# Optimization experiments

Measured on AMD Instinct MI355X. Metric: run time of the kernel, lower is better.

Reference implementation:

```python
import jax, jax.numpy as jnp
import numpy as np

N_NODES = 100000
N_EDGES = 2000000
N_GRAPHS = 1000
DIM = 32
NUM_FEATURES = 7
NUM_CLASSES = 2
BN_EPS = 1e-5


def setup_inputs() -> dict:
    key = jax.random.key(0)
    ks = jax.random.split(key, 24)
    inp = {
        "x": jax.random.normal(ks[0], (N_NODES, NUM_FEATURES), dtype=jnp.float32),
        "edge_index": jax.random.randint(ks[1], (2, N_EDGES), 0, N_NODES, dtype=jnp.int64),
        "batch": jnp.sort(jax.random.randint(ks[2], (N_NODES,), 0, N_GRAPHS, dtype=jnp.int64)),
        "conv1_W1": jax.random.normal(ks[3], (NUM_FEATURES, DIM), dtype=jnp.float32) * 0.3,
        "conv1_b1": jax.random.normal(ks[4], (DIM,), dtype=jnp.float32) * 0.1,
        "conv1_W2": jax.random.normal(ks[5], (DIM, DIM), dtype=jnp.float32) * 0.15,
        "conv1_b2": jax.random.normal(ks[6], (DIM,), dtype=jnp.float32) * 0.1,
        "convs_W1": jax.random.normal(ks[7], (4, DIM, DIM), dtype=jnp.float32) * 0.15,
        "convs_b1": jax.random.normal(ks[8], (4, DIM), dtype=jnp.float32) * 0.1,
        "convs_W2": jax.random.normal(ks[9], (4, DIM, DIM), dtype=jnp.float32) * 0.15,
        "convs_b2": jax.random.normal(ks[10], (4, DIM), dtype=jnp.float32) * 0.1,
        "bn_gamma": jax.random.uniform(ks[11], (5, DIM), dtype=jnp.float32, minval=0.5, maxval=1.5),
        "bn_beta": jax.random.normal(ks[12], (5, DIM), dtype=jnp.float32) * 0.1,
        "bn_mean": jax.random.normal(ks[13], (5, DIM), dtype=jnp.float32) * 0.1,
        "bn_var": jax.random.uniform(ks[14], (5, DIM), dtype=jnp.float32, minval=0.5, maxval=1.5),
        "fc1_W": jax.random.normal(ks[15], (DIM, DIM), dtype=jnp.float32) * 0.15,
        "fc1_b": jax.random.normal(ks[16], (DIM,), dtype=jnp.float32) * 0.1,
        "fc2_W": jax.random.normal(ks[17], (DIM, NUM_CLASSES), dtype=jnp.float32) * 0.15,
        "fc2_b": jax.random.normal(ks[18], (NUM_CLASSES,), dtype=jnp.float32) * 0.1,
    }
    return inp


def _gin_conv(h, src, dst, W1, b1, W2, b2):
    # GINConv with eps=0: nn((1+eps)*x + sum_{j in N(i)} x_j)
    agg = jax.ops.segment_sum(h[src], dst, num_segments=N_NODES)
    z = h + agg
    z = jnp.maximum(z @ W1 + b1, 0.0)
    return z @ W2 + b2


def _bn_eval(h, gamma, beta, mean, var):
    return (h - mean) * jax.lax.rsqrt(var + BN_EPS) * gamma + beta


def reference(x, edge_index, batch,
              conv1_W1, conv1_b1, conv1_W2, conv1_b2,
              convs_W1, convs_b1, convs_W2, convs_b2,
              bn_gamma, bn_beta, bn_mean, bn_var,
              fc1_W, fc1_b, fc2_W, fc2_b):
    src, dst = edge_index[0], edge_index[1]
    h = _gin_conv(x, src, dst, conv1_W1, conv1_b1, conv1_W2, conv1_b2)
    h = jnp.maximum(h, 0.0)
    h = _bn_eval(h, bn_gamma[0], bn_beta[0], bn_mean[0], bn_var[0])
    for i in range(4):  # conv2..conv5
        h = _gin_conv(h, src, dst, convs_W1[i], convs_b1[i], convs_W2[i], convs_b2[i])
        h = jnp.maximum(h, 0.0)
        h = _bn_eval(h, bn_gamma[i + 1], bn_beta[i + 1], bn_mean[i + 1], bn_var[i + 1])
    # global add pool over graphs
    g = jax.ops.segment_sum(h, batch, num_segments=N_GRAPHS)  # [G, DIM]
    g = jnp.maximum(g @ fc1_W + fc1_b, 0.0)
    # dropout: eval mode -> identity
    logits = g @ fc2_W + fc2_b
    return jax.nn.log_softmax(logits, axis=-1)
```

## Files before the change

### kernel.cpp

```cpp
#include <hip/hip_runtime.h>

#define N_NODES  100000
#define N_EDGES  2000000
#define N_GRAPHS 1000
#define NFEAT    7
#define BN_EPS   1e-5f
#define MAXDEG   64

#define BSH      7
#define NBKT     782
#define BCAP     3584
#define E_PER_BLK 4096

__device__ __forceinline__ unsigned bf16_rne(float f) {
  unsigned u = __float_as_uint(f);
  return (u + 0x7FFFu + ((u >> 16) & 1u)) >> 16;
}
__device__ __forceinline__ float bf_lo(unsigned u) { return __uint_as_float(u << 16); }
__device__ __forceinline__ float bf_hi(unsigned u) { return __uint_as_float(u & 0xFFFF0000u); }

__global__ __launch_bounds__(1024) void b1_bucket(const int* __restrict__ src,
                                                  const int* __restrict__ dst,
                                                  int* __restrict__ gCur,
                                                  unsigned* __restrict__ ebuf) {
  __shared__ int hist[NBKT], base[NBKT];
  int tid = threadIdx.x;
  for (int i = tid; i < NBKT; i += 1024) hist[i] = 0;
  __syncthreads();
  unsigned pk[4];
  int bo[4];
  int e0 = blockIdx.x * E_PER_BLK;
#pragma unroll
  for (int k = 0; k < 4; ++k) {
    int e = e0 + k * 1024 + tid;
    if (e < N_EDGES) {
      int d = dst[e], s = src[e];
      int b = d >> BSH;
      int off = atomicAdd(&hist[b], 1);
      pk[k] = ((unsigned)(d & 127) << 17) | (unsigned)s;
      bo[k] = (b << 17) | off;
    } else {
      bo[k] = -1;
    }
  }
  __syncthreads();
  for (int i = tid; i < NBKT; i += 1024)
    base[i] = hist[i] ? atomicAdd(&gCur[i], hist[i]) : 0;
  __syncthreads();
#pragma unroll
  for (int k = 0; k < 4; ++k) {
    if (bo[k] >= 0) {
      int b = bo[k] >> 17, off = bo[k] & 0x1FFFF;
      int p = base[b] + off;
      if (p < BCAP) ebuf[(size_t)b * BCAP + p] = pk[k];
    }
  }
}

__global__ __launch_bounds__(512) void b2_csr(const unsigned* __restrict__ ebuf,
                                              const int* __restrict__ gCnt,
                                              int* __restrict__ cnt,
                                              int* __restrict__ csr) {
  __shared__ int hist[128];
  __shared__ int stage[128 * MAXDEG];
  int b = blockIdx.x, tid = threadIdx.x;
  if (tid < 128) hist[tid] = 0;
  __syncthreads();
  int n = gCnt[b];
  if (n > BCAP) n = BCAP;
  const unsigned* eb = ebuf + (size_t)b * BCAP;
  for (int i = tid; i < n; i += 512) {
    unsigned pk = eb[i];
    int dloc = (int)(pk >> 17);
    int slot = atomicAdd(&hist[dloc], 1);
    if (slot < MAXDEG) stage[(dloc << 6) + slot] = (int)(pk & 0x1FFFFu);
  }
  __syncthreads();
  if (tid < 128) {
    int gnode = (b << BSH) + tid;
    if (gnode < N_NODES) cnt[gnode] = hist[tid];
  }
  const int4* st4 = (const int4*)stage;
  int4* dst4 = (int4*)(csr + (size_t)b * (128 * MAXDEG));
  for (int i = tid; i < 128 * MAXDEG / 4; i += 512) dst4[i] = st4[i];
}

__global__ __launch_bounds__(256) void xcvt_kernel(const float* __restrict__ x,
                                                   unsigned* __restrict__ xc) {
  int i = blockIdx.x * 256 + threadIdx.x;
  if (i >= N_NODES * 4) return;
  int n = i >> 2, p = i & 3;
  float lo = x[n * 7 + 2 * p];
  float hi = (2 * p + 1 < 7) ? x[n * 7 + 2 * p + 1] : 0.f;
  xc[i] = bf16_rne(lo) | (bf16_rne(hi) << 16);
}

__global__ __launch_bounds__(256) void gin1(
    const unsigned short* __restrict__ xc16, const int* __restrict__ cnt,
    const int* __restrict__ csr,
    const float* __restrict__ W1, const float* __restrict__ b1,
    const float* __restrict__ W2, const float* __restrict__ b2,
    const float* __restrict__ gamma, const float* __restrict__ beta,
    const float* __restrict__ mean, const float* __restrict__ var,
    unsigned short* __restrict__ hout16) {
  __shared__ __align__(16) float zsA[4][8], zsB[4][8];
  __shared__ __align__(16) float tsA[4][32], tsB[4][32];
  int tid = threadIdx.x;
  int w = __builtin_amdgcn_readfirstlane(tid >> 6);
  int lane = tid & 63;
  int grp = lane >> 2;
  int ch  = lane & 3;
  int half = lane >> 5, j = lane & 31;

  float wr1[4], wr2[16];
#pragma unroll
  for (int i = 0; i < 4; ++i) {
    int k = half * 4 + i;
    wr1[i] = (k < 7) ? W1[k * 32 + j] : 0.f;
  }
#pragma unroll
  for (int i = 0; i < 16; ++i) wr2[i] = W2[(half * 16 + i) * 32 + j];
  float vb1 = b1[j], vb2 = b2[j];
  float sc = gamma[j] * rsqrtf(var[j] + BN_EPS);
  float sh = beta[j] - mean[j] * sc;

  const unsigned* xc32 = (const unsigned*)xc16;

  const int NW = gridDim.x * 4;
  const int NPAIR = N_NODES / 2;
  for (int pr = blockIdx.x * 4 + w; pr < NPAIR; pr += NW) {
    int n0 = 2 * pr, n1 = n0 + 1;
    int d0 = cnt[n0];
    int d1 = cnt[n1];
    if (d0 > 63) d0 = 63;
    if (d1 > 63) d1 = 63;
    int dE0 = d0 + 1, dE1 = d1 + 1;

    int idx0 = (lane < d0) ? csr[n0 * MAXDEG + lane] : n0;
    int idx1 = (lane < d1) ? csr[n1 * MAXDEG + lane] : n1;

    unsigned vA[4], vB[4];
#pragma unroll
    for (int s = 0; s < 4; ++s) {
      int sidA = __shfl(idx0, s * 16 + grp);
      vA[s] = xc32[(size_t)sidA * 4 + ch];
    }
#pragma unroll
    for (int s = 0; s < 4; ++s) {
      int sidB = __shfl(idx1, s * 16 + grp);
      vB[s] = xc32[(size_t)sidB * 4 + ch];
    }

    float a0 = 0.f, a1 = 0.f;
    float c0 = 0.f, c1 = 0.f;
#pragma unroll
    for (int s = 0; s < 4; ++s) {
      int e = s * 16 + grp;
      if (e < dE0) { a0 += bf_lo(vA[s]); a1 += bf_hi(vA[s]); }
      if (e < dE1) { c0 += bf_lo(vB[s]); c1 += bf_hi(vB[s]); }
    }
#pragma unroll
    for (int m = 4; m <= 32; m <<= 1) {
      a0 += __shfl_xor(a0, m); a1 += __shfl_xor(a1, m);
      c0 += __shfl_xor(c0, m); c1 += __shfl_xor(c1, m);
    }
    if (grp == 0) {
      float2 za = {a0, a1};
      float2 zc = {c0, c1};
      *(float2*)&zsA[w][ch * 2] = za;
      *(float2*)&zsB[w][ch * 2] = zc;
    }

    float tp = half ? 0.f : vb1;
    {
      const float4* zp = (const float4*)&zsA[w][half * 4];
      float4 z0 = zp[0];
      tp = fmaf(z0.x, wr1[0], tp); tp = fmaf(z0.y, wr1[1], tp);
      tp = fmaf(z0.z, wr1[2], tp); tp = fmaf(z0.w, wr1[3], tp);
    }
    tp += __shfl_xor(tp, 32);
    tp = fmaxf(tp, 0.f);
    if (!half) tsA[w][j] = tp;

    float op = half ? 0.f : vb2;
    {
      const float4* tpp = (const float4*)&tsA[w][half * 16];
      float4 t0 = tpp[0], t1 = tpp[1], t2 = tpp[2], t3 = tpp[3];
      op = fmaf(t0.x, wr2[0], op);  op = fmaf(t0.y, wr2[1], op);
      op = fmaf(t0.z, wr2[2], op);  op = fmaf(t0.w, wr2[3], op);
      op = fmaf(t1.x, wr2[4], op);  op = fmaf(t1.y, wr2[5], op);
      op = fmaf(t1.z, wr2[6], op);  op = fmaf(t1.w, wr2[7], op);
      op = fmaf(t2.x, wr2[8], op);  op = fmaf(t2.y, wr2[9], op);
      op = fmaf(t2.z, wr2[10], op); op = fmaf(t2.w, wr2[11], op);
      op = fmaf(t3.x, wr2[12], op); op = fmaf(t3.y, wr2[13], op);
      op = fmaf(t3.z, wr2[14], op); op = fmaf(t3.w, wr2[15], op);
    }
    op += __shfl_xor(op, 32);
    if (!half) {
      op = fmaxf(op, 0.f) * sc + sh;
      float hi = __shfl(op, j | 1);
      if ((j & 1) == 0) {
        unsigned pk = bf16_rne(op) | (bf16_rne(hi) << 16);
        ((unsigned*)hout16)[n0 * 16 + (j >> 1)] = pk;
      }
    }

    float tq = half ? 0.f : vb1;
    {
      const float4* zp = (const float4*)&zsB[w][half * 4];
      float4 z0 = zp[0];
      tq = fmaf(z0.x, wr1[0], tq); tq = fmaf(z0.y, wr1[1], tq);
      tq = fmaf(z0.z, wr1[2], tq); tq = fmaf(z0.w, wr1[3], tq);
    }
    tq += __shfl_xor(tq, 32);
    tq = fmaxf(tq, 0.f);
    if (!half) tsB[w][j] = tq;

    float oq = half ? 0.f : vb2;
    {
      const float4* tpp = (const float4*)&tsB[w][half * 16];
      float4 t0 = tpp[0], t1 = tpp[1], t2 = tpp[2], t3 = tpp[3];
      oq = fmaf(t0.x, wr2[0], oq);  oq = fmaf(t0.y, wr2[1], oq);
      oq = fmaf(t0.z, wr2[2], oq);  oq = fmaf(t0.w, wr2[3], oq);
      oq = fmaf(t1.x, wr2[4], oq);  oq = fmaf(t1.y, wr2[5], oq);
      oq = fmaf(t1.z, wr2[6], oq);  oq = fmaf(t1.w, wr2[7], oq);
      oq = fmaf(t2.x, wr2[8], oq);  oq = fmaf(t2.y, wr2[9], oq);
      oq = fmaf(t2.z, wr2[10], oq); oq = fmaf(t2.w, wr2[11], oq);
      oq = fmaf(t3.x, wr2[12], oq); oq = fmaf(t3.y, wr2[13], oq);
      oq = fmaf(t3.z, wr2[14], oq); oq = fmaf(t3.w, wr2[15], oq);
    }
    oq += __shfl_xor(oq, 32);
    if (!half) {
      oq = fmaxf(oq, 0.f) * sc + sh;
      float hi = __shfl(oq, j | 1);
      if ((j & 1) == 0) {
        unsigned pk = bf16_rne(oq) | (bf16_rne(hi) << 16);
        ((unsigned*)hout16)[n1 * 16 + (j >> 1)] = pk;
      }
    }
  }
}

__global__ __launch_bounds__(256) void gin_layer32(
    const unsigned short* __restrict__ hin16, const int* __restrict__ cnt,
    const int* __restrict__ csr,
    const float* __restrict__ W1, const float* __restrict__ b1,
    const float* __restrict__ W2, const float* __restrict__ b2,
    const float* __restrict__ gamma, const float* __restrict__ beta,
    const float* __restrict__ mean, const float* __restrict__ var,
    unsigned short* __restrict__ hout16) {
  __shared__ __align__(16) float zsA[4][32], tsA[4][32];
  __shared__ __align__(16) float zsB[4][32], tsB[4][32];
  int tid = threadIdx.x;
  int w = __builtin_amdgcn_readfirstlane(tid >> 6);
  int lane = tid & 63;
  int grp = lane >> 3;
  int ch  = lane & 7;
  int half = lane >> 5, j = lane & 31;

  float wr1[16], wr2[16];
#pragma unroll
  for (int i = 0; i < 16; ++i) wr1[i] = W1[(half * 16 + i) * 32 + j];
#pragma unroll
  for (int i = 0; i < 16; ++i) wr2[i] = W2[(half * 16 + i) * 32 + j];
  float vb1 = b1[j], vb2 = b2[j];
  float sc = gamma[j] * rsqrtf(var[j] + BN_EPS);
  float sh = beta[j] - mean[j] * sc;

  const int NW = gridDim.x * 4;
  const int NPAIR = N_NODES / 2;
  for (int pr = blockIdx.x * 4 + w; pr < NPAIR; pr += NW) {
    int n0 = 2 * pr, n1 = n0 + 1;
    int d0 = cnt[n0];
    int d1 = cnt[n1];
    if (d0 > 63) d0 = 63;
    if (d1 > 63) d1 = 63;
    int dE0 = d0 + 1, dE1 = d1 + 1;

    int idx0 = (lane < d0) ? csr[n0 * MAXDEG + lane] : n0;
    int idx1 = (lane < d1) ? csr[n1 * MAXDEG + lane] : n1;

    uint2 vA[8], vB[8];
#pragma unroll
    for (int s = 0; s < 8; ++s) {
      int sidA = __shfl(idx0, s * 8 + grp);
      vA[s] = *(const uint2*)(hin16 + (size_t)sidA * 32 + ch * 4);
    }
#pragma unroll
    for (int s = 0; s < 8; ++s) {
      int sidB = __shfl(idx1, s * 8 + grp);
      vB[s] = *(const uint2*)(hin16 + (size_t)sidB * 32 + ch * 4);
    }

    float a0 = 0.f, a1 = 0.f, a2 = 0.f, a3 = 0.f;
    float c0 = 0.f, c1 = 0.f, c2 = 0.f, c3 = 0.f;
#pragma unroll
    for (int s = 0; s < 8; ++s) {
      int e = s * 8 + grp;
      if (e < dE0) {
        a0 += bf_lo(vA[s].x); a1 += bf_hi(vA[s].x);
        a2 += bf_lo(vA[s].y); a3 += bf_hi(vA[s].y);
      }
      if (e < dE1) {
        c0 += bf_lo(vB[s].x); c1 += bf_hi(vB[s].x);
        c2 += bf_lo(vB[s].y); c3 += bf_hi(vB[s].y);
      }
    }
#pragma unroll
    for (int m = 8; m <= 32; m <<= 1) {
      a0 += __shfl_xor(a0, m); a1 += __shfl_xor(a1, m);
      a2 += __shfl_xor(a2, m); a3 += __shfl_xor(a3, m);
      c0 += __shfl_xor(c0, m); c1 += __shfl_xor(c1, m);
      c2 += __shfl_xor(c2, m); c3 += __shfl_xor(c3, m);
    }
    if (grp == 0) {
      float4 za = {a0, a1, a2, a3};
      float4 zc = {c0, c1, c2, c3};
      *(float4*)&zsA[w][ch * 4] = za;
      *(float4*)&zsB[w][ch * 4] = zc;
    }

    float tp = half ? 0.f : vb1;
    {
      const float4* zp = (const float4*)&zsA[w][half * 16];
      float4 q0 = zp[0], q1 = zp[1], q2 = zp[2], q3 = zp[3];
      tp = fmaf(q0.x, wr1[0], tp);  tp = fmaf(q0.y, wr1[1], tp);
      tp = fmaf(q0.z, wr1[2], tp);  tp = fmaf(q0.w, wr1[3], tp);
      tp = fmaf(q1.x, wr1[4], tp);  tp = fmaf(q1.y, wr1[5], tp);
      tp = fmaf(q1.z, wr1[6], tp);  tp = fmaf(q1.w, wr1[7], tp);
      tp = fmaf(q2.x, wr1[8], tp);  tp = fmaf(q2.y, wr1[9], tp);
      tp = fmaf(q2.z, wr1[10], tp); tp = fmaf(q2.w, wr1[11], tp);
      tp = fmaf(q3.x, wr1[12], tp); tp = fmaf(q3.y, wr1[13], tp);
      tp = fmaf(q3.z, wr1[14], tp); tp = fmaf(q3.w, wr1[15], tp);
    }
    tp += __shfl_xor(tp, 32);
    tp = fmaxf(tp, 0.f);
    if (!half) tsA[w][j] = tp;

    float op = half ? 0.f : vb2;
    {
      const float4* tpp = (const float4*)&tsA[w][half * 16];
      float4 q0 = tpp[0], q1 = tpp[1], q2 = tpp[2], q3 = tpp[3];
      op = fmaf(q0.x, wr2[0], op);  op = fmaf(q0.y, wr2[1], op);
      op = fmaf(q0.z, wr2[2], op);  op = fmaf(q0.w, wr2[3], op);
      op = fmaf(q1.x, wr2[4], op);  op = fmaf(q1.y, wr2[5], op);
      op = fmaf(q1.z, wr2[6], op);  op = fmaf(q1.w, wr2[7], op);
      op = fmaf(q2.x, wr2[8], op);  op = fmaf(q2.y, wr2[9], op);
      op = fmaf(q2.z, wr2[10], op); op = fmaf(q2.w, wr2[11], op);
      op = fmaf(q3.x, wr2[12], op); op = fmaf(q3.y, wr2[13], op);
      op = fmaf(q3.z, wr2[14], op); op = fmaf(q3.w, wr2[15], op);
    }
    op += __shfl_xor(op, 32);
    if (!half) {
      op = fmaxf(op, 0.f) * sc + sh;
      float hi = __shfl(op, j | 1);
      if ((j & 1) == 0) {
        unsigned pk = bf16_rne(op) | (bf16_rne(hi) << 16);
        ((unsigned*)hout16)[n0 * 16 + (j >> 1)] = pk;
      }
    }

    float tq = half ? 0.f : vb1;
    {
      const float4* zp = (const float4*)&zsB[w][half * 16];
      float4 q0 = zp[0], q1 = zp[1], q2 = zp[2], q3 = zp[3];
      tq = fmaf(q0.x, wr1[0], tq);  tq = fmaf(q0.y, wr1[1], tq);
      tq = fmaf(q0.z, wr1[2], tq);  tq = fmaf(q0.w, wr1[3], tq);
      tq = fmaf(q1.x, wr1[4], tq);  tq = fmaf(q1.y, wr1[5], tq);
      tq = fmaf(q1.z, wr1[6], tq);  tq = fmaf(q1.w, wr1[7], tq);
      tq = fmaf(q2.x, wr1[8], tq);  tq = fmaf(q2.y, wr1[9], tq);
      tq = fmaf(q2.z, wr1[10], tq); tq = fmaf(q2.w, wr1[11], tq);
      tq = fmaf(q3.x, wr1[12], tq); tq = fmaf(q3.y, wr1[13], tq);
      tq = fmaf(q3.z, wr1[14], tq); tq = fmaf(q3.w, wr1[15], tq);
    }
    tq += __shfl_xor(tq, 32);
    tq = fmaxf(tq, 0.f);
    if (!half) tsB[w][j] = tq;

    float oq = half ? 0.f : vb2;
    {
      const float4* tpp = (const float4*)&tsB[w][half * 16];
      float4 q0 = tpp[0], q1 = tpp[1], q2 = tpp[2], q3 = tpp[3];
      oq = fmaf(q0.x, wr2[0], oq);  oq = fmaf(q0.y, wr2[1], oq);
      oq = fmaf(q0.z, wr2[2], oq);  oq = fmaf(q0.w, wr2[3], oq);
      oq = fmaf(q1.x, wr2[4], oq);  oq = fmaf(q1.y, wr2[5], oq);
      oq = fmaf(q1.z, wr2[6], oq);  oq = fmaf(q1.w, wr2[7], oq);
      oq = fmaf(q2.x, wr2[8], oq);  oq = fmaf(q2.y, wr2[9], oq);
      oq = fmaf(q2.z, wr2[10], oq); oq = fmaf(q2.w, wr2[11], oq);
      oq = fmaf(q3.x, wr2[12], oq); oq = fmaf(q3.y, wr2[13], oq);
      oq = fmaf(q3.z, wr2[14], oq); oq = fmaf(q3.w, wr2[15], oq);
    }
    oq += __shfl_xor(oq, 32);
    if (!half) {
      oq = fmaxf(oq, 0.f) * sc + sh;
      float hi = __shfl(oq, j | 1);
      if ((j & 1) == 0) {
        unsigned pk = bf16_rne(oq) | (bf16_rne(hi) << 16);
        ((unsigned*)hout16)[n1 * 16 + (j >> 1)] = pk;
      }
    }
  }
}

__global__ __launch_bounds__(256) void pool_kernel(const unsigned short* __restrict__ h16,
                                                   const int* __restrict__ batch,
                                                   float* __restrict__ g) {
  __shared__ int s_lo, s_hi;
  __shared__ float red[8][33];
  int gr = blockIdx.x;
  if (threadIdx.x == 0) {
    int lo = 0, hi = N_NODES;
    while (lo < hi) { int m = (lo + hi) >> 1; if (batch[m] < gr) lo = m + 1; else hi = m; }
    s_lo = lo;
  } else if (threadIdx.x == 1) {
    int lo = 0, hi = N_NODES;
    while (lo < hi) { int m = (lo + hi) >> 1; if (batch[m] < gr + 1) lo = m + 1; else hi = m; }
    s_hi = lo;
  }
  __syncthreads();
  int lo = s_lo, hi = s_hi;
  int j = threadIdx.x & 31;
  int nd = threadIdx.x >> 5;
  float acc = 0.f;
  for (int n = lo + nd; n < hi; n += 8)
    acc += __uint_as_float((unsigned)h16[n * 32 + j] << 16);
  red[nd][j] = acc;
  __syncthreads();
  if (threadIdx.x < 32) {
    float s = 0.f;
#pragma unroll
    for (int r = 0; r < 8; ++r) s += red[r][j];
    g[gr * 32 + j] = s;
  }
}

__global__ __launch_bounds__(256) void head_kernel(
    const float* __restrict__ g, const float* __restrict__ W1, const float* __restrict__ b1,
    const float* __restrict__ W2, const float* __restrict__ b2, float* __restrict__ out) {
  __shared__ float sW1[1024], sb1[32];
  __shared__ float sW2[64], sb2[2];
  __shared__ float zb[8][33], tb[8][33], lb[8][2];
  int tid = threadIdx.x;
  for (int i = tid; i < 1024; i += 256) sW1[i] = W1[i];
  if (tid < 64) sW2[tid] = W2[tid];
  if (tid < 32) sb1[tid] = b1[tid];
  if (tid < 2) sb2[tid] = b2[tid];
  int nd = tid >> 5;
  int gr = blockIdx.x * 8 + nd;
  int j = tid & 31;
  __syncthreads();
  float z = (gr < N_GRAPHS) ? g[gr * 32 + j] : 0.f;
  zb[nd][j] = z;
  __syncthreads();
  float t = sb1[j];
#pragma unroll
  for (int k = 0; k < 32; ++k) t = fmaf(zb[nd][k], sW1[k * 32 + j], t);
  t = fmaxf(t, 0.f);
  tb[nd][j] = t;
  __syncthreads();
  if (j < 2) {
    float l = sb2[j];
#pragma unroll
    for (int k = 0; k < 32; ++k) l = fmaf(tb[nd][k], sW2[k * 2 + j], l);
    lb[nd][j] = l;
  }
  __syncthreads();
  if (gr < N_GRAPHS && j < 2) {
    float l0 = lb[nd][0], l1 = lb[nd][1];
    float m = fmaxf(l0, l1);
    float lse = m + logf(expf(l0 - m) + expf(l1 - m));
    out[gr * 2 + j] = lb[nd][j] - lse;
  }
}

extern "C" void kernel_launch(void* const* d_in, const int* in_sizes, int n_in,
                              void* d_out, int out_size, void* d_ws, size_t ws_size,
                              hipStream_t stream) {
  const float* x     = (const float*)d_in[0];
  const int*   eidx  = (const int*)d_in[1];
  const int*   batch = (const int*)d_in[2];
  const float* c1W1  = (const float*)d_in[3];
  const float* c1b1  = (const float*)d_in[4];
  const float* c1W2  = (const float*)d_in[5];
  const float* c1b2  = (const float*)d_in[6];
  const float* csW1  = (const float*)d_in[7];
  const float* csb1  = (const float*)d_in[8];
  const float* csW2  = (const float*)d_in[9];
  const float* csb2  = (const float*)d_in[10];
  const float* bng   = (const float*)d_in[11];
  const float* bnb   = (const float*)d_in[12];
  const float* bnm   = (const float*)d_in[13];
  const float* bnv   = (const float*)d_in[14];
  const float* fc1W  = (const float*)d_in[15];
  const float* fc1b  = (const float*)d_in[16];
  const float* fc2W  = (const float*)d_in[17];
  const float* fc2b  = (const float*)d_in[18];
  float* out = (float*)d_out;

  const int* src = eidx;
  const int* dst = eidx + N_EDGES;

  char* p = (char*)d_ws;
  unsigned short* hA16 = (unsigned short*)p; p += (size_t)N_NODES * 32 * 2;
  unsigned short* hB16 = (unsigned short*)p; p += (size_t)N_NODES * 32 * 2;
  int*      cnt  = (int*)p;      p += (size_t)N_NODES * 4;
  int*      csr  = (int*)p;      p += (size_t)NBKT * 128 * MAXDEG * 4;
  unsigned* ebuf = (unsigned*)p; p += (size_t)NBKT * BCAP * 4;
  int*      gCur = (int*)p;      p += 1024 * 4;
  float*    g    = (float*)p;    p += (size_t)N_GRAPHS * 32 * 4;
  unsigned* xc = ebuf;

  hipMemsetAsync(gCur, 0, 1024 * 4, stream);
  b1_bucket<<<(N_EDGES + E_PER_BLK - 1) / E_PER_BLK, 1024, 0, stream>>>(src, dst, gCur, ebuf);
  b2_csr<<<NBKT, 512, 0, stream>>>(ebuf, gCur, cnt, csr);

  xcvt_kernel<<<(N_NODES * 4 + 255) / 256, 256, 0, stream>>>(x, xc);

  gin1<<<2048, 256, 0, stream>>>(
      (const unsigned short*)xc, cnt, csr, c1W1, c1b1, c1W2, c1b2,
      bng, bnb, bnm, bnv, hA16);

  unsigned short* cur = hA16;
  unsigned short* nxt = hB16;
  for (int i = 0; i < 4; ++i) {
    gin_layer32<<<2048, 256, 0, stream>>>(
        cur, cnt, csr,
        csW1 + (size_t)i * 1024, csb1 + (size_t)i * 32,
        csW2 + (size_t)i * 1024, csb2 + (size_t)i * 32,
        bng + (size_t)(i + 1) * 32, bnb + (size_t)(i + 1) * 32,
        bnm + (size_t)(i + 1) * 32, bnv + (size_t)(i + 1) * 32, nxt);
    unsigned short* tmp = cur; cur = nxt; nxt = tmp;
  }

  pool_kernel<<<N_GRAPHS, 256, 0, stream>>>(cur, batch, g);
  head_kernel<<<(N_GRAPHS + 7) / 8, 256, 0, stream>>>(g, fc1W, fc1b, fc2W, fc2b, out);
}
```

Measured before the change: 366.3 us.

## Split GIN layer into separate aggregation and MLP kernels via fp32 buffer

The fused gather-plus-MLP layer kernel is split into an aggregation kernel that writes fp32 z rows to a global buffer and a tiled MLP kernel that processes 64 nodes per block from shared memory. Dropping the weight registers from the gather kernel is meant to improve occupancy and latency hiding for the irregular neighbor loads. In exchange, each layer adds an fp32 write and read of the full node-feature matrix plus an extra launch. Workspace buffers are re-aliased so the z buffer reuses the edge-bucket scratch.

```diff
diff --git a/kernel.cpp b/kernel.cpp
--- a/kernel.cpp
+++ b/kernel.cpp
@@ -241,31 +241,14 @@
   }
 }
 
-__global__ __launch_bounds__(256) void gin_layer32(
+__global__ __launch_bounds__(256) void gin32_agg(
     const unsigned short* __restrict__ hin16, const int* __restrict__ cnt,
-    const int* __restrict__ csr,
-    const float* __restrict__ W1, const float* __restrict__ b1,
-    const float* __restrict__ W2, const float* __restrict__ b2,
-    const float* __restrict__ gamma, const float* __restrict__ beta,
-    const float* __restrict__ mean, const float* __restrict__ var,
-    unsigned short* __restrict__ hout16) {
-  __shared__ __align__(16) float zsA[4][32], tsA[4][32];
-  __shared__ __align__(16) float zsB[4][32], tsB[4][32];
+    const int* __restrict__ csr, float* __restrict__ z) {
   int tid = threadIdx.x;
   int w = __builtin_amdgcn_readfirstlane(tid >> 6);
   int lane = tid & 63;
   int grp = lane >> 3;
   int ch  = lane & 7;
-  int half = lane >> 5, j = lane & 31;
-
-  float wr1[16], wr2[16];
-#pragma unroll
-  for (int i = 0; i < 16; ++i) wr1[i] = W1[(half * 16 + i) * 32 + j];
-#pragma unroll
-  for (int i = 0; i < 16; ++i) wr2[i] = W2[(half * 16 + i) * 32 + j];
-  float vb1 = b1[j], vb2 = b2[j];
-  float sc = gamma[j] * rsqrtf(var[j] + BN_EPS);
-  float sh = beta[j] - mean[j] * sc;
 
   const int NW = gridDim.x * 4;
   const int NPAIR = N_NODES / 2;
@@ -316,13 +299,55 @@
     if (grp == 0) {
       float4 za = {a0, a1, a2, a3};
       float4 zc = {c0, c1, c2, c3};
-      *(float4*)&zsA[w][ch * 4] = za;
-      *(float4*)&zsB[w][ch * 4] = zc;
-    }
-
+      *(float4*)(z + (size_t)n0 * 32 + ch * 4) = za;
+      *(float4*)(z + (size_t)n1 * 32 + ch * 4) = zc;
+    }
+  }
+}
+
+__global__ __launch_bounds__(256) void mlp32(
+    const float* __restrict__ z,
+    const float* __restrict__ W1, const float* __restrict__ b1,
+    const float* __restrict__ W2, const float* __restrict__ b2,
+    const float* __restrict__ gamma, const float* __restrict__ beta,
+    const float* __restrict__ mean, const float* __restrict__ var,
+    unsigned short* __restrict__ hout16) {
+  __shared__ __align__(16) float zs[64][36];
+  __shared__ __align__(16) float ts[4][32];
+  int tid = threadIdx.x;
+  int w = __builtin_amdgcn_readfirstlane(tid >> 6);
+  int lane = tid & 63;
+  int half = lane >> 5, j = lane & 31;
+
+  float wr1[16], wr2[16];
+#pragma unroll
+  for (int i = 0; i < 16; ++i) wr1[i] = W1[(half * 16 + i) * 32 + j];
+#pragma unroll
+  for (int i = 0; i < 16; ++i) wr2[i] = W2[(half * 16 + i) * 32 + j];
+  float vb1 = b1[j], vb2 = b2[j];
+  float sc = gamma[j] * rsqrtf(var[j] + BN_EPS);
+  float sh = beta[j] - mean[j] * sc;
+
+  int base = blockIdx.x * 64;
+  {
+    int r = tid >> 2, c = (tid & 3) * 8;
+    int node = base + r;
+    float4 f0 = {0.f, 0.f, 0.f, 0.f}, f1 = f0;
+    if (node < N_NODES) {
+      const float4* zp = (const float4*)(z + (size_t)node * 32 + c);
+      f0 = zp[0]; f1 = zp[1];
+    }
+    *(float4*)&zs[r][c]     = f0;
+    *(float4*)&zs[r][c + 4] = f1;
+  }
+  __syncthreads();
+
+  for (int p = 0; p < 16; ++p) {
+    int nloc = (w << 4) + p;
+    int node = base + nloc;
     float tp = half ? 0.f : vb1;
     {
-      const float4* zp = (const float4*)&zsA[w][half * 16];
+      const float4* zp = (const float4*)&zs[nloc][half * 16];
       float4 q0 = zp[0], q1 = zp[1], q2 = zp[2], q3 = zp[3];
       tp = fmaf(q0.x, wr1[0], tp);  tp = fmaf(q0.y, wr1[1], tp);
       tp = fmaf(q0.z, wr1[2], tp);  tp = fmaf(q0.w, wr1[3], tp);
@@ -335,11 +360,10 @@
     }
     tp += __shfl_xor(tp, 32);
     tp = fmaxf(tp, 0.f);
-    if (!half) tsA[w][j] = tp;
-
+    if (!half) ts[w][j] = tp;
     float op = half ? 0.f : vb2;
     {
-      const float4* tpp = (const float4*)&tsA[w][half * 16];
+      const float4* tpp = (const float4*)&ts[w][half * 16];
       float4 q0 = tpp[0], q1 = tpp[1], q2 = tpp[2], q3 = tpp[3];
       op = fmaf(q0.x, wr2[0], op);  op = fmaf(q0.y, wr2[1], op);
       op = fmaf(q0.z, wr2[2], op);  op = fmaf(q0.w, wr2[3], op);
@@ -351,52 +375,12 @@
       op = fmaf(q3.z, wr2[14], op); op = fmaf(q3.w, wr2[15], op);
     }
     op += __shfl_xor(op, 32);
-    if (!half) {
+    if (!half && node < N_NODES) {
       op = fmaxf(op, 0.f) * sc + sh;
       float hi = __shfl(op, j | 1);
       if ((j & 1) == 0) {
         unsigned pk = bf16_rne(op) | (bf16_rne(hi) << 16);
-        ((unsigned*)hout16)[n0 * 16 + (j >> 1)] = pk;
-      }
-    }
-
-    float tq = half ? 0.f : vb1;
-    {
-      const float4* zp = (const float4*)&zsB[w][half * 16];
-      float4 q0 = zp[0], q1 = zp[1], q2 = zp[2], q3 = zp[3];
-      tq = fmaf(q0.x, wr1[0], tq);  tq = fmaf(q0.y, wr1[1], tq);
-      tq = fmaf(q0.z, wr1[2], tq);  tq = fmaf(q0.w, wr1[3], tq);
-      tq = fmaf(q1.x, wr1[4], tq);  tq = fmaf(q1.y, wr1[5], tq);
-      tq = fmaf(q1.z, wr1[6], tq);  tq = fmaf(q1.w, wr1[7], tq);
-      tq = fmaf(q2.x, wr1[8], tq);  tq = fmaf(q2.y, wr1[9], tq);
-      tq = fmaf(q2.z, wr1[10], tq); tq = fmaf(q2.w, wr1[11], tq);
-      tq = fmaf(q3.x, wr1[12], tq); tq = fmaf(q3.y, wr1[13], tq);
-      tq = fmaf(q3.z, wr1[14], tq); tq = fmaf(q3.w, wr1[15], tq);
-    }
-    tq += __shfl_xor(tq, 32);
-    tq = fmaxf(tq, 0.f);
-    if (!half) tsB[w][j] = tq;
-
-    float oq = half ? 0.f : vb2;
-    {
-      const float4* tpp = (const float4*)&tsB[w][half * 16];
-      float4 q0 = tpp[0], q1 = tpp[1], q2 = tpp[2], q3 = tpp[3];
-      oq = fmaf(q0.x, wr2[0], oq);  oq = fmaf(q0.y, wr2[1], oq);
-      oq = fmaf(q0.z, wr2[2], oq);  oq = fmaf(q0.w, wr2[3], oq);
-      oq = fmaf(q1.x, wr2[4], oq);  oq = fmaf(q1.y, wr2[5], oq);
-      oq = fmaf(q1.z, wr2[6], oq);  oq = fmaf(q1.w, wr2[7], oq);
-      oq = fmaf(q2.x, wr2[8], oq);  oq = fmaf(q2.y, wr2[9], oq);
-      oq = fmaf(q2.z, wr2[10], oq); oq = fmaf(q2.w, wr2[11], oq);
-      oq = fmaf(q3.x, wr2[12], oq); oq = fmaf(q3.y, wr2[13], oq);
-      oq = fmaf(q3.z, wr2[14], oq); oq = fmaf(q3.w, wr2[15], oq);
-    }
-    oq += __shfl_xor(oq, 32);
-    if (!half) {
-      oq = fmaxf(oq, 0.f) * sc + sh;
-      float hi = __shfl(oq, j | 1);
-      if ((j & 1) == 0) {
-        unsigned pk = bf16_rne(oq) | (bf16_rne(hi) << 16);
-        ((unsigned*)hout16)[n1 * 16 + (j >> 1)] = pk;
+        ((unsigned*)hout16)[node * 16 + (j >> 1)] = pk;
       }
     }
   }
@@ -505,10 +489,11 @@
   unsigned short* hB16 = (unsigned short*)p; p += (size_t)N_NODES * 32 * 2;
   int*      cnt  = (int*)p;      p += (size_t)N_NODES * 4;
   int*      csr  = (int*)p;      p += (size_t)NBKT * 128 * MAXDEG * 4;
-  unsigned* ebuf = (unsigned*)p; p += (size_t)NBKT * BCAP * 4;
-  int*      gCur = (int*)p;      p += 1024 * 4;
+  float*    zbuf = (float*)p;    p += (size_t)N_NODES * 32 * 4;
+  unsigned* ebuf = (unsigned*)zbuf;
+  int*      gCur = (int*)((char*)zbuf + (size_t)NBKT * BCAP * 4);
   float*    g    = (float*)p;    p += (size_t)N_GRAPHS * 32 * 4;
-  unsigned* xc = ebuf;
+  unsigned* xc = (unsigned*)hB16;
 
   hipMemsetAsync(gCur, 0, 1024 * 4, stream);
   b1_bucket<<<(N_EDGES + E_PER_BLK - 1) / E_PER_BLK, 1024, 0, stream>>>(src, dst, gCur, ebuf);
@@ -523,8 +508,9 @@
   unsigned short* cur = hA16;
   unsigned short* nxt = hB16;
   for (int i = 0; i < 4; ++i) {
-    gin_layer32<<<2048, 256, 0, stream>>>(
-        cur, cnt, csr,
+    gin32_agg<<<2048, 256, 0, stream>>>(cur, cnt, csr, zbuf);
+    mlp32<<<(N_NODES + 63) / 64, 256, 0, stream>>>(
+        zbuf,
         csW1 + (size_t)i * 1024, csb1 + (size_t)i * 32,
         csW2 + (size_t)i * 1024, csb2 + (size_t)i * 32,
         bng + (size_t)(i + 1) * 32, bnb + (size_t)(i + 1) * 32,
```

Result: slower. 378.9 us (+3.4%).

## Gather 16-byte neighbor rows per lane and reduce via DPP/permlane swaps

Applied to the files above, without the earlier changes.

Reworks the lane mapping in the GIN layer gather so each lane loads a 16-byte uint4 covering 8 bf16 features, with 16 edge slots across 4 iterations instead of 8 slots of 8-byte loads. Each lane now reads its CSR index directly rather than broadcasting it via shuffles. Cross-lane reductions and the bf16 pair packing switch from ds_bpermute-based __shfl to DPP moves and permlane32_swap. This aims to cut shuffle/LDS traffic and issue fewer, wider memory requests. In exchange it doubles the accumulator registers and relies on a specific lane permutation for the DPP reduction to stay correct.

```diff
diff --git a/kernel.cpp b/kernel.cpp
--- a/kernel.cpp
+++ b/kernel.cpp
@@ -18,6 +18,22 @@
 }
 __device__ __forceinline__ float bf_lo(unsigned u) { return __uint_as_float(u << 16); }
 __device__ __forceinline__ float bf_hi(unsigned u) { return __uint_as_float(u & 0xFFFF0000u); }
+
+template <int CTRL>
+__device__ __forceinline__ float dppmov(float x) {
+  return __uint_as_float((unsigned)__builtin_amdgcn_update_dpp(
+      (int)__float_as_uint(x), (int)__float_as_uint(x), CTRL, 0xf, 0xf, false));
+}
+#define DPP_XOR1  0xB1
+#define DPP_XOR2  0x4E
+#define DPP_ROR8  0x128
+#define DPP_HI    0xF5
+
+__device__ __forceinline__ float sumxor32(float x) {
+  auto r = __builtin_amdgcn_permlane32_swap(__float_as_uint(x), __float_as_uint(x),
+                                            false, false);
+  return __uint_as_float(r[0]) + __uint_as_float(r[1]);
+}
 
 __global__ __launch_bounds__(1024) void b1_bucket(const int* __restrict__ src,
                                                   const int* __restrict__ dst,
@@ -254,8 +270,8 @@
   int tid = threadIdx.x;
   int w = __builtin_amdgcn_readfirstlane(tid >> 6);
   int lane = tid & 63;
-  int grp = lane >> 3;
-  int ch  = lane & 7;
+  int sl = (lane & 3) | ((lane >> 1) & 4) | ((lane >> 2) & 8);
+  int ch = ((lane >> 2) & 1) | ((lane >> 3) & 2);
   int half = lane >> 5, j = lane & 31;
 
   float wr1[16], wr2[16];
@@ -277,47 +293,49 @@
     if (d1 > 63) d1 = 63;
     int dE0 = d0 + 1, dE1 = d1 + 1;
 
-    int idx0 = (lane < d0) ? csr[n0 * MAXDEG + lane] : n0;
-    int idx1 = (lane < d1) ? csr[n1 * MAXDEG + lane] : n1;
-
-    uint2 vA[8], vB[8];
-#pragma unroll
-    for (int s = 0; s < 8; ++s) {
-      int sidA = __shfl(idx0, s * 8 + grp);
-      vA[s] = *(const uint2*)(hin16 + (size_t)sidA * 32 + ch * 4);
-    }
-#pragma unroll
-    for (int s = 0; s < 8; ++s) {
-      int sidB = __shfl(idx1, s * 8 + grp);
-      vB[s] = *(const uint2*)(hin16 + (size_t)sidB * 32 + ch * 4);
-    }
-
     float a0 = 0.f, a1 = 0.f, a2 = 0.f, a3 = 0.f;
+    float a4 = 0.f, a5 = 0.f, a6 = 0.f, a7 = 0.f;
     float c0 = 0.f, c1 = 0.f, c2 = 0.f, c3 = 0.f;
-#pragma unroll
-    for (int s = 0; s < 8; ++s) {
-      int e = s * 8 + grp;
+    float c4 = 0.f, c5 = 0.f, c6 = 0.f, c7 = 0.f;
+#pragma unroll
+    for (int s = 0; s < 4; ++s) {
+      int e = s * 16 + sl;
+      int i0 = csr[n0 * MAXDEG + e];
+      int i1 = csr[n1 * MAXDEG + e];
+      int sidA = (e < d0) ? i0 : n0;
+      int sidB = (e < d1) ? i1 : n1;
+      uint4 vA = *(const uint4*)(hin16 + (size_t)sidA * 32 + ch * 8);
+      uint4 vB = *(const uint4*)(hin16 + (size_t)sidB * 32 + ch * 8);
       if (e < dE0) {
-        a0 += bf_lo(vA[s].x); a1 += bf_hi(vA[s].x);
-        a2 += bf_lo(vA[s].y); a3 += bf_hi(vA[s].y);
+        a0 += bf_lo(vA.x); a1 += bf_hi(vA.x);
+        a2 += bf_lo(vA.y); a3 += bf_hi(vA.y);
+        a4 += bf_lo(vA.z); a5 += bf_hi(vA.z);
+        a6 += bf_lo(vA.w); a7 += bf_hi(vA.w);
       }
       if (e < dE1) {
-        c0 += bf_lo(vB[s].x); c1 += bf_hi(vB[s].x);
-        c2 += bf_lo(vB[s].y); c3 += bf_hi(vB[s].y);
+        c0 += bf_lo(vB.x); c1 += bf_hi(vB.x);
+        c2 += bf_lo(vB.y); c3 += bf_hi(vB.y);
+        c4 += bf_lo(vB.z); c5 += bf_hi(vB.z);
+        c6 += bf_lo(vB.w); c7 += bf_hi(vB.w);
       }
     }
-#pragma unroll
-    for (int m = 8; m <= 32; m <<= 1) {
-      a0 += __shfl_xor(a0, m); a1 += __shfl_xor(a1, m);
-      a2 += __shfl_xor(a2, m); a3 += __shfl_xor(a3, m);
-      c0 += __shfl_xor(c0, m); c1 += __shfl_xor(c1, m);
-      c2 += __shfl_xor(c2, m); c3 += __shfl_xor(c3, m);
-    }
-    if (grp == 0) {
-      float4 za = {a0, a1, a2, a3};
-      float4 zc = {c0, c1, c2, c3};
-      *(float4*)&zsA[w][ch * 4] = za;
-      *(float4*)&zsB[w][ch * 4] = zc;
+#define RED(x) x += dppmov<DPP_XOR1>(x); x += dppmov<DPP_XOR2>(x); \
+               x += dppmov<DPP_ROR8>(x); x = sumxor32(x);
+    RED(a0) RED(a1) RED(a2) RED(a3) RED(a4) RED(a5) RED(a6) RED(a7)
+    RED(c0) RED(c1) RED(c2) RED(c3) RED(c4) RED(c5) RED(c6) RED(c7)
+#undef RED
+
+    if (sl == 0) {
+      float4 za0 = {a0, a1, a2, a3};
+      float4 za1 = {a4, a5, a6, a7};
+      *(float4*)&zsA[w][ch * 8]     = za0;
+      *(float4*)&zsA[w][ch * 8 + 4] = za1;
+    }
+    if (sl == 1) {
+      float4 zc0 = {c0, c1, c2, c3};
+      float4 zc1 = {c4, c5, c6, c7};
+      *(float4*)&zsB[w][ch * 8]     = zc0;
+      *(float4*)&zsB[w][ch * 8 + 4] = zc1;
     }
 
     float tp = half ? 0.f : vb1;
@@ -333,7 +351,7 @@
       tp = fmaf(q3.x, wr1[12], tp); tp = fmaf(q3.y, wr1[13], tp);
       tp = fmaf(q3.z, wr1[14], tp); tp = fmaf(q3.w, wr1[15], tp);
     }
-    tp += __shfl_xor(tp, 32);
+    tp = sumxor32(tp);
     tp = fmaxf(tp, 0.f);
     if (!half) tsA[w][j] = tp;
 
@@ -350,11 +368,11 @@
       op = fmaf(q3.x, wr2[12], op); op = fmaf(q3.y, wr2[13], op);
       op = fmaf(q3.z, wr2[14], op); op = fmaf(q3.w, wr2[15], op);
     }
-    op += __shfl_xor(op, 32);
-    if (!half) {
-      op = fmaxf(op, 0.f) * sc + sh;
-      float hi = __shfl(op, j | 1);
-      if ((j & 1) == 0) {
+    op = sumxor32(op);
+    op = fmaxf(op, 0.f) * sc + sh;
+    {
+      float hi = dppmov<DPP_HI>(op);
+      if (!half && (j & 1) == 0) {
         unsigned pk = bf16_rne(op) | (bf16_rne(hi) << 16);
         ((unsigned*)hout16)[n0 * 16 + (j >> 1)] = pk;
       }
@@ -373,7 +391,7 @@
       tq = fmaf(q3.x, wr1[12], tq); tq = fmaf(q3.y, wr1[13], tq);
       tq = fmaf(q3.z, wr1[14], tq); tq = fmaf(q3.w, wr1[15], tq);
     }
-    tq += __shfl_xor(tq, 32);
+    tq = sumxor32(tq);
     tq = fmaxf(tq, 0.f);
     if (!half) tsB[w][j] = tq;
 
@@ -390,11 +408,11 @@
       oq = fmaf(q3.x, wr2[12], oq); oq = fmaf(q3.y, wr2[13], oq);
       oq = fmaf(q3.z, wr2[14], oq); oq = fmaf(q3.w, wr2[15], oq);
     }
-    oq += __shfl_xor(oq, 32);
-    if (!half) {
-      oq = fmaxf(oq, 0.f) * sc + sh;
-      float hi = __shfl(oq, j | 1);
-      if ((j & 1) == 0) {
+    oq = sumxor32(oq);
+    oq = fmaxf(oq, 0.f) * sc + sh;
+    {
+      float hi = dppmov<DPP_HI>(oq);
+      if (!half && (j & 1) == 0) {
         unsigned pk = bf16_rne(oq) | (bf16_rne(hi) << 16);
         ((unsigned*)hout16)[n1 * 16 + (j >> 1)] = pk;
       }
@@ -510,7 +528,7 @@
   float*    g    = (float*)p;    p += (size_t)N_GRAPHS * 32 * 4;
   unsigned* xc = ebuf;
 
-  hipMemsetAsync(gCur, 0, 1024 * 4, stream);
+  (void)hipMemsetAsync(gCur, 0, 1024 * 4, stream);
   b1_bucket<<<(N_EDGES + E_PER_BLK - 1) / E_PER_BLK, 1024, 0, stream>>>(src, dst, gCur, ebuf);
   b2_csr<<<NBKT, 512, 0, stream>>>(ebuf, gCur, cnt, csr);
 
```

After: 407.2 us. 1.11x slower.
